# Optimization experiments

Hardware: AMD Instinct MI355X
Metric: run time of the kernel (lower is better)

The kernel has to match this reference:

```python
import jax, jax.numpy as jnp
import numpy as np

B, S, H = 64, 2048, 1024
NEG = -1e10


def setup_inputs() -> dict:
    key = jax.random.key(0)
    k1, k2, k3, k4, k5, k6 = jax.random.split(key, 6)
    scale = 1.0 / np.sqrt(2 * H)
    return {
        "decoder_hidden": jax.random.normal(k1, (B, H), dtype=jnp.float32),
        "encoder_outputs": jax.random.normal(k2, (B, S, H), dtype=jnp.float32),
        "mask": jax.random.randint(k3, (B, S), 0, 2, dtype=jnp.int32),
        "W_attn": jax.random.normal(k4, (2 * H, H), dtype=jnp.float32) * scale,
        "b_attn": jax.random.normal(k5, (H,), dtype=jnp.float32) * scale,
        "v_w": jax.random.normal(k6, (H,), dtype=jnp.float32) * (1.0 / np.sqrt(H)),
    }


def reference(decoder_hidden, encoder_outputs, mask, W_attn, b_attn, v_w):
    # concat((dec_rep, enc), -1) @ W_attn == dec @ W_attn[:H] + enc @ W_attn[H:]
    Wd, We = W_attn[:H], W_attn[H:]
    dec_proj = decoder_hidden @ Wd            # [B, H]
    enc_proj = jnp.einsum('bsh,hk->bsk', encoder_outputs, We)  # [B, S, H]
    energy = jnp.tanh(dec_proj[:, None, :] + enc_proj + b_attn)  # [B, S, H]
    attention = jnp.einsum('bsh,h->bs', energy, v_w)             # [B, S]
    attention = jnp.where(mask == 1, NEG, attention)
    return jax.nn.softmax(attention, axis=1)
```

## Files before the change

kernel.cpp:

```cpp
#include <hip/hip_runtime.h>
#include <hip/hip_bf16.h>
#include <stdint.h>

#define HD   1024
#define BB   64
#define SS   2048
#define MT   (BB*SS)
#define NEGV -10000000000.0f

typedef __attribute__((ext_vector_type(8))) short bf16x8;
typedef __attribute__((ext_vector_type(4))) float f32x4;
typedef __attribute__((ext_vector_type(4))) int   i32x4;

__device__ __forceinline__ void gll16(const void* g, void* l) {
  __builtin_amdgcn_global_load_lds((const __attribute__((address_space(1))) void*)g,
                                   (__attribute__((address_space(3))) void*)l, 16, 0, 0);
}

__device__ __forceinline__ float tanh_fast(float x) {
  float e = __expf(2.0f * x);
  return 1.0f - 2.0f / (e + 1.0f);
}

__global__ void prep_we(const float* __restrict__ Wattn, __hip_bfloat16* __restrict__ out) {
  __shared__ float st[64][132];
  int tid = threadIdx.x;
  int nt = blockIdx.x >> 4, kc = blockIdx.x & 15;
  const float* src = Wattn + (size_t)(HD + kc*64)*HD + nt*128;
  #pragma unroll 4
  for (int i = 0; i < 32; ++i) {
    int s = i*256 + tid;
    int kk = s >> 7, nn = s & 127;
    st[kk][nn] = src[(size_t)kk*HD + nn];
  }
  __syncthreads();
  size_t base = (size_t)blockIdx.x * 8192;
  #pragma unroll 4
  for (int i = 0; i < 32; ++i) {
    int lin = i*256 + tid;
    int nl = lin >> 6, j = (lin >> 3) & 7, e = lin & 7;
    int kk = ((j ^ (nl & 7)) << 3) + e;
    out[base + lin] = __float2bfloat16(st[kk][nl]);
  }
}

__global__ void prep_dpb(const float* __restrict__ dec, const float* __restrict__ Wattn,
                         const float* __restrict__ battn, float* __restrict__ dpb) {
  __shared__ float dh[HD];
  int tid = threadIdx.x;
  int b = blockIdx.y;
  int n = blockIdx.x*256 + tid;
  #pragma unroll
  for (int i = 0; i < 4; ++i) dh[i*256 + tid] = dec[b*HD + i*256 + tid];
  __syncthreads();
  float acc = battn[n];
  #pragma unroll 8
  for (int h = 0; h < HD; ++h) acc += dh[h] * Wattn[(size_t)h*HD + n];
  dpb[b*HD + n] = acc;
}

__global__ void __launch_bounds__(256) gemm_fused(
    const float* __restrict__ E, const __hip_bfloat16* __restrict__ Wt,
    const float* __restrict__ dpb, const float* __restrict__ vw,
    float* __restrict__ logits) {
  __shared__ __align__(16) short Al[128*72];
  __shared__ __align__(16) short Bl[128*64];
  __shared__ float red[128];

  int tid = threadIdx.x;
  int lane = tid & 63, wid = tid >> 6;
  int wm = wid & 1, wn = wid >> 1;
  int bm = blockIdx.x >> 3, bn = blockIdx.x & 7;
  int m0 = bm << 7, n0 = bn << 7;
  int lane15 = lane & 15, kg = lane >> 4;

  f32x4 acc[4][4];
  #pragma unroll
  for (int a = 0; a < 4; ++a)
    #pragma unroll
    for (int c = 0; c < 4; ++c) acc[a][c] = (f32x4){0.f, 0.f, 0.f, 0.f};

  for (int kc = 0; kc < 16; ++kc) {
    const char* bt = (const char*)Wt + ((size_t)(bn*16 + kc) * 8192) * 2;
    #pragma unroll
    for (int i = 0; i < 4; ++i) {
      int segbase = (wid*4 + i) * 64;
      gll16(bt + (size_t)(segbase + lane)*16, (char*)Bl + segbase*16);
    }
    const float* Eg = E + (m0*HD + kc*64);
    #pragma unroll
    for (int i = 0; i < 8; ++i) {
      int s = i*256 + tid;
      int r = s >> 4, q = s & 15;
      f32x4 v = *(const f32x4*)(Eg + r*HD + q*4);
      union { __hip_bfloat162 h[2]; unsigned long long u; } cv;
      cv.h[0] = __float22bfloat162_rn(make_float2(v.x, v.y));
      cv.h[1] = __float22bfloat162_rn(make_float2(v.z, v.w));
      *(unsigned long long*)&Al[r*72 + q*4] = cv.u;
    }
    __syncthreads();
    #pragma unroll
    for (int kh = 0; kh < 2; ++kh) {
      bf16x8 af[4], bfr[4];
      #pragma unroll
      for (int mf = 0; mf < 4; ++mf) {
        int row = wm*64 + mf*16 + lane15;
        af[mf] = *(const bf16x8*)&Al[row*72 + kh*32 + kg*8];
      }
      #pragma unroll
      for (int nf = 0; nf < 4; ++nf) {
        int nl = wn*64 + nf*16 + lane15;
        int jj = kh*4 + kg;
        bfr[nf] = *(const bf16x8*)&Bl[nl*64 + ((jj ^ (nl & 7)) << 3)];
      }
      #pragma unroll
      for (int mf = 0; mf < 4; ++mf)
        #pragma unroll
        for (int nf = 0; nf < 4; ++nf)
          acc[mf][nf] = __builtin_amdgcn_mfma_f32_16x16x32_bf16(af[mf], bfr[nf], acc[mf][nf], 0, 0, 0);
    }
    __syncthreads();
  }

  int bidx = m0 >> 11;
  float dpv[4], vwv[4];
  #pragma unroll
  for (int nf = 0; nf < 4; ++nf) {
    int n = n0 + wn*64 + nf*16 + lane15;
    dpv[nf] = dpb[bidx*HD + n];
    vwv[nf] = vw[n];
  }
  if (tid < 128) red[tid] = 0.0f;
  __syncthreads();
  #pragma unroll
  for (int mf = 0; mf < 4; ++mf) {
    #pragma unroll
    for (int r = 0; r < 4; ++r) {
      float s = 0.0f;
      #pragma unroll
      for (int nf = 0; nf < 4; ++nf) {
        float x = acc[mf][nf][r] + dpv[nf];
        s += tanh_fast(x) * vwv[nf];
      }
      s += __shfl_xor(s, 1); s += __shfl_xor(s, 2);
      s += __shfl_xor(s, 4); s += __shfl_xor(s, 8);
      if (lane15 == 0) atomicAdd(&red[wm*64 + mf*16 + kg*4 + r], s);
    }
  }
  __syncthreads();
  if (tid < 128) atomicAdd(&logits[m0 + tid], red[tid]);
}

__global__ void softmax_k(const float* __restrict__ logits, const int* __restrict__ mask,
                          float* __restrict__ out) {
  __shared__ float smax[4];
  __shared__ float ssum[4];
  int tid = threadIdx.x, lane = tid & 63, wid = tid >> 6;
  int b = blockIdx.x;
  const float* lg = logits + b*SS;
  const int*   mk = mask   + b*SS;
  f32x4 l0 = *(const f32x4*)(lg + tid*8);
  f32x4 l1 = *(const f32x4*)(lg + tid*8 + 4);
  i32x4 q0 = *(const i32x4*)(mk + tid*8);
  i32x4 q1 = *(const i32x4*)(mk + tid*8 + 4);
  float v[8];
  v[0] = (q0.x == 1) ? NEGV : l0.x;  v[1] = (q0.y == 1) ? NEGV : l0.y;
  v[2] = (q0.z == 1) ? NEGV : l0.z;  v[3] = (q0.w == 1) ? NEGV : l0.w;
  v[4] = (q1.x == 1) ? NEGV : l1.x;  v[5] = (q1.y == 1) ? NEGV : l1.y;
  v[6] = (q1.z == 1) ? NEGV : l1.z;  v[7] = (q1.w == 1) ? NEGV : l1.w;
  float mx = v[0];
  #pragma unroll
  for (int i = 1; i < 8; ++i) mx = fmaxf(mx, v[i]);
  #pragma unroll
  for (int m = 1; m <= 32; m <<= 1) mx = fmaxf(mx, __shfl_xor(mx, m));
  if (lane == 0) smax[wid] = mx;
  __syncthreads();
  mx = fmaxf(fmaxf(smax[0], smax[1]), fmaxf(smax[2], smax[3]));
  float s = 0.0f;
  #pragma unroll
  for (int i = 0; i < 8; ++i) { v[i] = __expf(v[i] - mx); s += v[i]; }
  #pragma unroll
  for (int m = 1; m <= 32; m <<= 1) s += __shfl_xor(s, m);
  if (lane == 0) ssum[wid] = s;
  __syncthreads();
  s = ssum[0] + ssum[1] + ssum[2] + ssum[3];
  float inv = 1.0f / s;
  f32x4 o0 = {v[0]*inv, v[1]*inv, v[2]*inv, v[3]*inv};
  f32x4 o1 = {v[4]*inv, v[5]*inv, v[6]*inv, v[7]*inv};
  *(f32x4*)(out + b*SS + tid*8)     = o0;
  *(f32x4*)(out + b*SS + tid*8 + 4) = o1;
}

extern "C" void kernel_launch(void* const* d_in, const int* in_sizes, int n_in,
                              void* d_out, int out_size, void* d_ws, size_t ws_size,
                              hipStream_t stream) {
  const float* dec   = (const float*)d_in[0];
  const float* enc   = (const float*)d_in[1];
  const int*   mask  = (const int*)  d_in[2];
  const float* Wattn = (const float*)d_in[3];
  const float* battn = (const float*)d_in[4];
  const float* vw    = (const float*)d_in[5];
  float* out = (float*)d_out;

  char* ws = (char*)d_ws;
  __hip_bfloat16* wet = (__hip_bfloat16*)ws;
  float* dpb    = (float*)(ws + (size_t)2*1024*1024);
  float* logits = (float*)(ws + (size_t)2*1024*1024 + 256*1024);

  prep_we <<<128, 256, 0, stream>>>(Wattn, wet);
  prep_dpb<<<dim3(4, 64), 256, 0, stream>>>(dec, Wattn, battn, dpb);
  hipMemsetAsync(logits, 0, (size_t)MT*sizeof(float), stream);
  gemm_fused<<<8192, 256, 0, stream>>>(enc, wet, dpb, vw, logits);
  softmax_k<<<BB, 256, 0, stream>>>(logits, mask, out);
}
```

Baseline: 1.254 ms.

## Pre-convert encoder outputs to swizzled bf16 tiles and remap GEMM blocks per XCD

Adds a prep_E pass that converts the fp32 encoder outputs once into bf16 tiles laid out in the same XOR-swizzled order as the weights. The GEMM can then stream A through global_load_lds instead of re-reading fp32 and converting in registers for each of the 8 N-tiles. Block indices are remapped so all N-tiles of one M-tile land on the same XCD, which should improve L2 reuse. prep_dpb is also split over K for more parallelism. The cost is an extra pass writing 256MB of bf16, and the new path only runs when the workspace is large enough; otherwise it falls back to the fp32 kernel.

```diff
diff --git a/kernel.cpp b/kernel.cpp
--- a/kernel.cpp
+++ b/kernel.cpp
@@ -21,6 +21,7 @@
   float e = __expf(2.0f * x);
   return 1.0f - 2.0f / (e + 1.0f);
 }
+
 
 __global__ void prep_we(const float* __restrict__ Wattn, __hip_bfloat16* __restrict__ out) {
   __shared__ float st[64][132];
@@ -44,22 +45,138 @@
   }
 }
 
+__global__ void prep_E(const float* __restrict__ E, __hip_bfloat16* __restrict__ out) {
+  int tid = threadIdx.x;
+  int mt = blockIdx.x >> 4, kc = blockIdx.x & 15;
+  const float* src = E + ((size_t)mt*128)*HD + kc*64;
+  __hip_bfloat16* dst = out + (size_t)blockIdx.x * 8192;
+  #pragma unroll
+  for (int i = 0; i < 4; ++i) {
+    int u = i*256 + tid;
+    int ml = u >> 3, j = u & 7;
+    int sk = ((j ^ (ml & 7)) << 3);
+    const float* p = src + (size_t)ml*HD + sk;
+    f32x4 v0 = *(const f32x4*)p;
+    f32x4 v1 = *(const f32x4*)(p + 4);
+    union { __hip_bfloat162 h[4]; i32x4 q; } cv;
+    cv.h[0] = __float22bfloat162_rn(make_float2(v0.x, v0.y));
+    cv.h[1] = __float22bfloat162_rn(make_float2(v0.z, v0.w));
+    cv.h[2] = __float22bfloat162_rn(make_float2(v1.x, v1.y));
+    cv.h[3] = __float22bfloat162_rn(make_float2(v1.z, v1.w));
+    *(i32x4*)(dst + (size_t)u*8) = cv.q;
+  }
+}
+
 __global__ void prep_dpb(const float* __restrict__ dec, const float* __restrict__ Wattn,
                          const float* __restrict__ battn, float* __restrict__ dpb) {
-  __shared__ float dh[HD];
+  __shared__ float red[4][64];
+  int b = blockIdx.y, n0 = blockIdx.x*64;
+  int nn = threadIdx.x & 63, kg = threadIdx.x >> 6;
+  const float* wp = Wattn + (size_t)(kg*256)*HD + n0 + nn;
+  const float* dp = dec + b*HD + kg*256;
+  float acc = 0.0f;
+  #pragma unroll 8
+  for (int h = 0; h < 256; ++h) acc += dp[h] * wp[(size_t)h*HD];
+  red[kg][nn] = acc;
+  __syncthreads();
+  if (threadIdx.x < 64) {
+    int n = n0 + threadIdx.x;
+    dpb[b*HD + n] = battn[n] + red[0][threadIdx.x] + red[1][threadIdx.x]
+                             + red[2][threadIdx.x] + red[3][threadIdx.x];
+  }
+}
+
+__device__ __forceinline__ void decode_bid(int bid, int& bm, int& bn) {
+  int x = bid & 7, r = bid >> 3;
+  bm = x*128 + (r >> 3);
+  bn = r & 7;
+}
+
+__global__ void __launch_bounds__(256) gemm_fused_bf(
+    const __hip_bfloat16* __restrict__ At, const __hip_bfloat16* __restrict__ Wt,
+    const float* __restrict__ dpb, const float* __restrict__ vw,
+    float* __restrict__ logits) {
+  __shared__ __align__(16) short Al[128*64];
+  __shared__ __align__(16) short Bl[128*64];
+  __shared__ float red[128];
+
   int tid = threadIdx.x;
-  int b = blockIdx.y;
-  int n = blockIdx.x*256 + tid;
-  #pragma unroll
-  for (int i = 0; i < 4; ++i) dh[i*256 + tid] = dec[b*HD + i*256 + tid];
-  __syncthreads();
-  float acc = battn[n];
-  #pragma unroll 8
-  for (int h = 0; h < HD; ++h) acc += dh[h] * Wattn[(size_t)h*HD + n];
-  dpb[b*HD + n] = acc;
-}
-
-__global__ void __launch_bounds__(256) gemm_fused(
+  int lane = tid & 63, wid = tid >> 6;
+  int wm = wid & 1, wn = wid >> 1;
+  int bm, bn; decode_bid(blockIdx.x, bm, bn);
+  int m0 = bm << 7, n0 = bn << 7;
+  int lane15 = lane & 15, kg = lane >> 4;
+
+  f32x4 acc[4][4];
+  #pragma unroll
+  for (int a = 0; a < 4; ++a)
+    #pragma unroll
+    for (int c = 0; c < 4; ++c) acc[a][c] = (f32x4){0.f, 0.f, 0.f, 0.f};
+
+  for (int kc = 0; kc < 16; ++kc) {
+    const char* at = (const char*)At + ((size_t)(bm*16 + kc) * 8192) * 2;
+    const char* bt = (const char*)Wt + ((size_t)(bn*16 + kc) * 8192) * 2;
+    #pragma unroll
+    for (int i = 0; i < 4; ++i) {
+      int segbase = (wid*4 + i) * 64;
+      gll16(at + (size_t)(segbase + lane)*16, (char*)Al + segbase*16);
+      gll16(bt + (size_t)(segbase + lane)*16, (char*)Bl + segbase*16);
+    }
+    __syncthreads();
+    #pragma unroll
+    for (int kh = 0; kh < 2; ++kh) {
+      bf16x8 af[4], bfr[4];
+      #pragma unroll
+      for (int mf = 0; mf < 4; ++mf) {
+        int row = wm*64 + mf*16 + lane15;
+        int jj = kh*4 + kg;
+        af[mf] = *(const bf16x8*)&Al[row*64 + ((jj ^ (row & 7)) << 3)];
+      }
+      #pragma unroll
+      for (int nf = 0; nf < 4; ++nf) {
+        int nl = wn*64 + nf*16 + lane15;
+        int jj = kh*4 + kg;
+        bfr[nf] = *(const bf16x8*)&Bl[nl*64 + ((jj ^ (nl & 7)) << 3)];
+      }
+      #pragma unroll
+      for (int mf = 0; mf < 4; ++mf)
+        #pragma unroll
+        for (int nf = 0; nf < 4; ++nf)
+          acc[mf][nf] = __builtin_amdgcn_mfma_f32_16x16x32_bf16(af[mf], bfr[nf], acc[mf][nf], 0, 0, 0);
+    }
+    __syncthreads();
+  }
+
+  int bidx = m0 >> 11;
+  float dpv[4], vwv[4];
+  #pragma unroll
+  for (int nf = 0; nf < 4; ++nf) {
+    int n = n0 + wn*64 + nf*16 + lane15;
+    dpv[nf] = dpb[bidx*HD + n];
+    vwv[nf] = vw[n];
+  }
+  if (tid < 128) red[tid] = 0.0f;
+  __syncthreads();
+  #pragma unroll
+  for (int mf = 0; mf < 4; ++mf) {
+    #pragma unroll
+    for (int r = 0; r < 4; ++r) {
+      float s = 0.0f;
+      #pragma unroll
+      for (int nf = 0; nf < 4; ++nf) {
+        float x = acc[mf][nf][r] + dpv[nf];
+        s += tanh_fast(x) * vwv[nf];
+      }
+      s += __shfl_xor(s, 1); s += __shfl_xor(s, 2);
+      s += __shfl_xor(s, 4); s += __shfl_xor(s, 8);
+      if (lane15 == 0) atomicAdd(&red[wm*64 + mf*16 + kg*4 + r], s);
+    }
+  }
+  __syncthreads();
+  if (tid < 128) atomicAdd(&logits[m0 + tid], red[tid]);
+}
+
+__global__ void __launch_bounds__(256) gemm_fused_f32(
     const float* __restrict__ E, const __hip_bfloat16* __restrict__ Wt,
     const float* __restrict__ dpb, const float* __restrict__ vw,
     float* __restrict__ logits) {
@@ -70,7 +187,7 @@
   int tid = threadIdx.x;
   int lane = tid & 63, wid = tid >> 6;
   int wm = wid & 1, wn = wid >> 1;
-  int bm = blockIdx.x >> 3, bn = blockIdx.x & 7;
+  int bm, bn; decode_bid(blockIdx.x, bm, bn);
   int m0 = bm << 7, n0 = bn << 7;
   int lane15 = lane & 15, kg = lane >> 4;
 
@@ -202,14 +319,31 @@
   const float* vw    = (const float*)d_in[5];
   float* out = (float*)d_out;
 
+  const size_t EBF_BYTES = (size_t)MT * HD * 2;
+  const size_t FAST_NEED = EBF_BYTES + (2u<<20) + (256u<<10) + (512u<<10);
+
   char* ws = (char*)d_ws;
-  __hip_bfloat16* wet = (__hip_bfloat16*)ws;
-  float* dpb    = (float*)(ws + (size_t)2*1024*1024);
-  float* logits = (float*)(ws + (size_t)2*1024*1024 + 256*1024);
-
-  prep_we <<<128, 256, 0, stream>>>(Wattn, wet);
-  prep_dpb<<<dim3(4, 64), 256, 0, stream>>>(dec, Wattn, battn, dpb);
-  hipMemsetAsync(logits, 0, (size_t)MT*sizeof(float), stream);
-  gemm_fused<<<8192, 256, 0, stream>>>(enc, wet, dpb, vw, logits);
-  softmax_k<<<BB, 256, 0, stream>>>(logits, mask, out);
-}
+  if (ws_size >= FAST_NEED) {
+    __hip_bfloat16* ebf = (__hip_bfloat16*)ws;
+    __hip_bfloat16* wet = (__hip_bfloat16*)(ws + EBF_BYTES);
+    float* dpb    = (float*)(ws + EBF_BYTES + (2u<<20));
+    float* logits = (float*)(ws + EBF_BYTES + (2u<<20) + (256u<<10));
+
+    prep_E <<<16384, 256, 0, stream>>>(enc, ebf);
+    prep_we<<<128, 256, 0, stream>>>(Wattn, wet);
+    prep_dpb<<<dim3(16, 64), 256, 0, stream>>>(dec, Wattn, battn, dpb);
+    hipMemsetAsync(logits, 0, (size_t)MT*sizeof(float), stream);
+    gemm_fused_bf<<<8192, 256, 0, stream>>>(ebf, wet, dpb, vw, logits);
+    softmax_k<<<BB, 256, 0, stream>>>(logits, mask, out);
+  } else {
+    __hip_bfloat16* wet = (__hip_bfloat16*)ws;
+    float* dpb    = (float*)(ws + (2u<<20));
+    float* logits = (float*)(ws + (2u<<20) + (256u<<10));
+
+    prep_we<<<128, 256, 0, stream>>>(Wattn, wet);
+    prep_dpb<<<dim3(16, 64), 256, 0, stream>>>(dec, Wattn, battn, dpb);
+    hipMemsetAsync(logits, 0, (size_t)MT*sizeof(float), stream);
+    gemm_fused_f32<<<8192, 256, 0, stream>>>(enc, wet, dpb, vw, logits);
+    softmax_k<<<BB, 256, 0, stream>>>(logits, mask, out);
+  }
+}
```

New measurement: 1.202 ms. 1.04x faster.
